# Optimization experiments

Measured on AMD Instinct MI355X. Metric: run time of the kernel, lower is better.

## Reference

```python
import jax, jax.numpy as jnp
import numpy as np

B, SQ, SKV = 4, 2048, 2048
IN_Q, IN_KV = 1024, 1024
H, D = 16, 64            # num_heads, hidden_channels (per-head dim)
OUT = 1024
ROPE_BASE = 4096.0


def _rope(x, base):
    # x: (..., items, D). Interleaved rotate-half RoPE over last dim.
    d = x.shape[-1]
    s = x.shape[-2]
    inv_freq = base ** (-jnp.arange(0, d, 2, dtype=x.dtype) / d)      # (D/2,)
    ang = jnp.arange(s, dtype=x.dtype)[:, None] * inv_freq[None, :]   # (S, D/2)
    cos = jnp.repeat(jnp.cos(ang), 2, axis=-1)                        # (S, D)
    sin = jnp.repeat(jnp.sin(ang), 2, axis=-1)
    xp = x.reshape(x.shape[:-1] + (d // 2, 2))
    x_rot = jnp.stack([-xp[..., 1], xp[..., 0]], axis=-1).reshape(x.shape)
    return x * cos + x_rot * sin


def setup_inputs() -> dict:
    key = jax.random.key(0)
    ks = jax.random.split(key, 8)
    sc = 0.02
    return {
        "q": jax.random.normal(ks[0], (B, SQ, IN_Q), jnp.float32),
        "kv": jax.random.normal(ks[1], (B, SKV, IN_KV), jnp.float32),
        # weights stored (in, out): y = x @ W + b  (equiv. to torch Linear)
        "Wq": jax.random.normal(ks[2], (IN_Q, H * D), jnp.float32) * sc,
        "bq": jnp.zeros((H * D,), jnp.float32),
        "Wkv": jax.random.normal(ks[3], (IN_KV, 2 * D), jnp.float32) * sc,
        "bkv": jnp.zeros((2 * D,), jnp.float32),
        "Wo": jax.random.normal(ks[4], (H * D, OUT), jnp.float32) * sc,
        "bo": jnp.zeros((OUT,), jnp.float32),
    }


def reference(q, kv, Wq, bq, Wkv, bkv, Wo, bo):
    # Q projection -> (B, H, SQ, D)
    qh = (q @ Wq + bq).reshape(B, SQ, H, D).transpose(0, 2, 1, 3)
    # KV projection (multi-query: single shared K/V head) -> (B, SKV, D) each
    kvp = kv @ Wkv + bkv
    k, v = kvp[..., :D], kvp[..., D:]
    # Rotary positional encoding on the item axis
    qh = _rope(qh, ROPE_BASE)
    k = _rope(k, ROPE_BASE)
    # Scaled dot-product attention with broadcast single-head K/V (MQA)
    scale = 1.0 / jnp.sqrt(jnp.asarray(D, qh.dtype))
    scores = jnp.einsum("bhqd,bkd->bhqk", qh, k) * scale   # (B,H,SQ,SKV)
    attn = jax.nn.softmax(scores, axis=-1)
    h = jnp.einsum("bhqk,bkd->bhqd", attn, v)              # (B,H,SQ,D)
    # Merge heads and output projection
    h = h.transpose(0, 2, 1, 3).reshape(B, SQ, H * D)
    return h @ Wo + bo
```

## Files before the change

kernel.cpp:

```cpp
#include <hip/hip_runtime.h>
#include <math.h>

typedef __bf16 bf16;
typedef __bf16 bf16x4 __attribute__((ext_vector_type(4)));
typedef __bf16 bf16x8 __attribute__((ext_vector_type(8)));
typedef float floatx4 __attribute__((ext_vector_type(4)));

#define MFMA16(a, b, c) __builtin_amdgcn_mfma_f32_16x16x32_bf16(a, b, c, 0, 0, 0)

#if __has_builtin(__builtin_amdgcn_exp2f)
#define EXP2F(x) __builtin_amdgcn_exp2f(x)
#else
#define EXP2F(x) exp2f(x)
#endif

constexpr int Bc = 4, SQc = 2048, SKVc = 2048, Hc = 16, Dc = 64;
#define QSCALE 0.18033688011112042f

__device__ __forceinline__ void glds16(const bf16* g, bf16* lds_base, int lane) {
#if __has_builtin(__builtin_amdgcn_global_load_lds)
  __builtin_amdgcn_global_load_lds(
      (const __attribute__((address_space(1))) void*)g,
      (__attribute__((address_space(3))) void*)lds_base, 16, 0, 0);
#else
  *(bf16x8*)(lds_base + 8 * lane) = *(const bf16x8*)g;
#endif
}

__global__ void cvt_bf16(const float* __restrict__ in, bf16* __restrict__ out) {
  const size_t i = ((size_t)blockIdx.x * 256 + threadIdx.x) * 4;
  const float4 v = *(const float4*)&in[i];
  bf16x4 o = {(bf16)v.x, (bf16)v.y, (bf16)v.z, (bf16)v.w};
  *(bf16x4*)&out[i] = o;
}

__global__ void rope_tab_build(float2* __restrict__ tab) {
  const int i = blockIdx.x * 256 + threadIdx.x;
  const int pos = i >> 5, f = i & 31;
  const float ang = (float)pos * exp2f(-0.375f * (float)f);
  float sn, cs;
  sincosf(ang, &sn, &cs);
  tab[i] = make_float2(cs, sn);
}

__global__ void transpose_cvt(const float* __restrict__ in, bf16* __restrict__ out,
                              int K, int N) {
  __shared__ bf16 T[64][72];
  const int tid = threadIdx.x;
  const int n0 = blockIdx.x * 64, k0 = blockIdx.y * 64;
  const int tr = tid >> 4, tc4 = (tid & 15) * 4;
#pragma unroll
  for (int i = 0; i < 4; i++) {
    const int k = tr + 16 * i;
    const float4 v = *(const float4*)&in[(size_t)(k0 + k) * N + n0 + tc4];
    T[tc4 + 0][k] = (bf16)v.x;
    T[tc4 + 1][k] = (bf16)v.y;
    T[tc4 + 2][k] = (bf16)v.z;
    T[tc4 + 3][k] = (bf16)v.w;
  }
  __syncthreads();
  const int nr = tid >> 2, kc = (tid & 3) * 8;
#pragma unroll
  for (int hf = 0; hf < 2; hf++)
    *(bf16x8*)&out[(size_t)(n0 + nr) * K + k0 + kc + 32 * hf] =
        *(const bf16x8*)&T[nr][kc + 32 * hf];
}

__device__ __forceinline__ void gemm_kloop(const bf16* __restrict__ A,
                                           const bf16* __restrict__ BT, int m0,
                                           int n0, int tid, int wave, int lane,
                                           int m, int g, bf16 (*As)[128 * 64],
                                           bf16 (*Bs)[128 * 64],
                                           floatx4 (*acc)[4], int mq, int nq) {
  const int r_ = tid >> 3, p_ = tid & 7;
  const bf16* pA[4];
  const bf16* pB[4];
#pragma unroll
  for (int q = 0; q < 4; q++) {
    const int r = r_ + q * 32;
    const int s = p_ ^ (r & 7);
    pA[q] = &A[(size_t)(m0 + r) * 1024 + 8 * s];
    pB[q] = &BT[(size_t)(n0 + r) * 1024 + 8 * s];
  }

#pragma unroll
  for (int q = 0; q < 4; q++) {
    glds16(pA[q], &As[0][(q * 4 + wave) * 512], lane);
    glds16(pB[q], &Bs[0][(q * 4 + wave) * 512], lane);
  }
  __syncthreads();

  for (int t = 0; t < 16; ++t) {
    const int cur = t & 1;
    if (t < 15) {
      const int k0 = 64 * (t + 1);
#pragma unroll
      for (int q = 0; q < 4; q++) {
        glds16(pA[q] + k0, &As[cur ^ 1][(q * 4 + wave) * 512], lane);
        glds16(pB[q] + k0, &Bs[cur ^ 1][(q * 4 + wave) * 512], lane);
      }
    }
    bf16x8 bb[4][2];
#pragma unroll
    for (int j = 0; j < 4; j++) {
      const int row = nq + 16 * j + m;
#pragma unroll
      for (int kh = 0; kh < 2; kh++)
        bb[j][kh] =
            *(const bf16x8*)&Bs[cur][row * 64 + 8 * ((g + 4 * kh) ^ (row & 7))];
    }
#pragma unroll
    for (int i = 0; i < 4; i++) {
      const int row = mq + 16 * i + m;
      const bf16x8 a0 = *(const bf16x8*)&As[cur][row * 64 + 8 * (g ^ (row & 7))];
      const bf16x8 a1 =
          *(const bf16x8*)&As[cur][row * 64 + 8 * ((g + 4) ^ (row & 7))];
#pragma unroll
      for (int j = 0; j < 4; j++) {
        acc[i][j] = MFMA16(a0, bb[j][0], acc[i][j]);
        acc[i][j] = MFMA16(a1, bb[j][1], acc[i][j]);
      }
    }
    __syncthreads();
  }
}

__global__ __launch_bounds__(256, 2) void gemm_qkv(
    const bf16* __restrict__ qA, const bf16* __restrict__ qBT,
    const float* __restrict__ qb, const bf16* __restrict__ kvA,
    const bf16* __restrict__ kvBT, const float* __restrict__ kvb,
    const float2* __restrict__ tab, bf16* __restrict__ qh,
    bf16* __restrict__ kko, bf16* __restrict__ vto) {
  __shared__ bf16 As[2][128 * 64];
  __shared__ bf16 Bs[2][128 * 64];

  const int tid = threadIdx.x, lane = tid & 63, wave = tid >> 6;
  const int m = lane & 15, g = lane >> 4;
  const int m0 = blockIdx.x * 128;
  const bool isQ = (blockIdx.y < 8);
  const int n0 = isQ ? blockIdx.y * 128 : 0;
  const bf16* A = isQ ? qA : kvA;
  const bf16* BT = isQ ? qBT : kvBT;
  const float* bias = isQ ? qb : kvb;
  const int mq = (wave >> 1) * 64, nq = (wave & 1) * 64;

  floatx4 z = {0.f, 0.f, 0.f, 0.f};
  floatx4 acc[4][4];
#pragma unroll
  for (int i = 0; i < 4; i++)
#pragma unroll
    for (int j = 0; j < 4; j++) acc[i][j] = z;

  gemm_kloop(A, BT, m0, n0, tid, wave, lane, m, g, As, Bs, acc, mq, nq);

  const int rq = 4 * g;
#pragma unroll
  for (int j = 0; j < 4; j++) {
    const int col = n0 + nq + 16 * j + m;
    const float bv = bias[col];
#pragma unroll
    for (int i = 0; i < 4; i++) {
#pragma unroll
      for (int r = 0; r < 4; r++) {
        const int row = m0 + mq + 16 * i + rq + r;
        float v = acc[i][j][r] + bv;
        const float vp = __shfl_xor(v, 1);
        if (isQ) {
          const int d = col & 63, hh = col >> 6;
          const int pos = row & (SQc - 1), b = row >> 11;
          const float2 cssn = tab[pos * 32 + (d >> 1)];
          const float res = (d & 1) ? (v * cssn.x + vp * cssn.y)
                                    : (v * cssn.x - vp * cssn.y);
          qh[(((size_t)(b * Hc + hh) * SQc) + pos) * Dc + d] = (bf16)(res * QSCALE);
        } else {
          const int pos = row & (SKVc - 1), b = row >> 11;
          const size_t fb = (size_t)b * (SKVc * Dc);
          if (col < 64) {
            const int d = col;
            const float2 cssn = tab[pos * 32 + (d >> 1)];
            const float res = (d & 1) ? (v * cssn.x + vp * cssn.y)
                                      : (v * cssn.x - vp * cssn.y);
            const int kc = (pos >> 4) * 2 + (d >> 5);
            const int kl = ((d >> 3) & 3) * 16 + (pos & 15);
            kko[fb + (size_t)kc * 512 + kl * 8 + (d & 7)] = (bf16)res;
          } else {
            const int d = col - 64;
            const int vc = (pos >> 6) * 8 + (d >> 4) * 2 + ((pos >> 5) & 1);
            const int vl = ((pos >> 3) & 3) * 16 + (d & 15);
            vto[fb + (size_t)vc * 512 + vl * 8 + (pos & 7)] = (bf16)v;
          }
        }
      }
    }
  }
}

__global__ __launch_bounds__(256, 2) void gemm_out(
    const bf16* __restrict__ A, const bf16* __restrict__ BT,
    const float* __restrict__ bias, float* __restrict__ out) {
  __shared__ bf16 As[2][128 * 64];
  __shared__ bf16 Bs[2][128 * 64];

  const int tid = threadIdx.x, lane = tid & 63, wave = tid >> 6;
  const int m = lane & 15, g = lane >> 4;
  const int m0 = blockIdx.x * 128, n0 = blockIdx.y * 128;
  const int mq = (wave >> 1) * 64, nq = (wave & 1) * 64;

  floatx4 z = {0.f, 0.f, 0.f, 0.f};
  floatx4 acc[4][4];
#pragma unroll
  for (int i = 0; i < 4; i++)
#pragma unroll
    for (int j = 0; j < 4; j++) acc[i][j] = z;

  gemm_kloop(A, BT, m0, n0, tid, wave, lane, m, g, As, Bs, acc, mq, nq);

  const int rq = 4 * g;
#pragma unroll
  for (int j = 0; j < 4; j++) {
    const int col = n0 + nq + 16 * j + m;
    const float bv = bias[col];
#pragma unroll
    for (int i = 0; i < 4; i++)
#pragma unroll
      for (int r = 0; r < 4; r++) {
        const int row = m0 + mq + 16 * i + rq + r;
        out[(size_t)row * 1024 + col] = acc[i][j][r] + bv;
      }
  }
}

__global__ __launch_bounds__(256, 2) void attn_v5(
    const bf16* __restrict__ qh, const bf16* __restrict__ kk,
    const bf16* __restrict__ vt, bf16* __restrict__ hout) {
  const int bid = blockIdx.x;
  const int qt = bid & 7, h = (bid >> 3) & 15, b = bid >> 7;
  const int tid = threadIdx.x, lane = tid & 63, wave = tid >> 6;
  const int m = lane & 15, g = lane >> 4;

  __shared__ bf16 Pb[4][4][16][68];

  const int q0 = qt * 256 + wave * 64;
  const bf16* qp = qh + (((size_t)(b * Hc + h) * SQc) + q0 + m) * Dc + 8 * g;
  bf16x8 bq[4][2];
#pragma unroll
  for (int s = 0; s < 4; s++) {
    bq[s][0] = *(const bf16x8*)(qp + (size_t)(16 * s) * Dc);
    bq[s][1] = *(const bf16x8*)(qp + (size_t)(16 * s) * Dc + 32);
  }

  const bf16 one = (bf16)1.0f;
  const bf16x8 ones = {one, one, one, one, one, one, one, one};

  floatx4 z = {0.f, 0.f, 0.f, 0.f};
  floatx4 accO[4][4];
  floatx4 lacc[4] = {z, z, z, z};
#pragma unroll
  for (int s = 0; s < 4; s++)
#pragma unroll
    for (int t = 0; t < 4; t++) accO[s][t] = z;

  const bf16* kfb = kk + (size_t)b * (SKVc * Dc) + 8 * lane;
  const bf16* vfb = vt + (size_t)b * (SKVc * Dc) + 8 * lane;

  bf16x8 kf[4][2];
#pragma unroll
  for (int c = 0; c < 4; c++) {
    kf[c][0] = *(const bf16x8*)(kfb + (size_t)(2 * c + 0) * 512);
    kf[c][1] = *(const bf16x8*)(kfb + (size_t)(2 * c + 1) * 512);
  }

  for (int it = 0; it < 32; ++it) {
    bf16x8 vf[4][2];
#pragma unroll
    for (int t = 0; t < 4; t++) {
      vf[t][0] = *(const bf16x8*)(vfb + (size_t)(it * 8 + 2 * t + 0) * 512);
      vf[t][1] = *(const bf16x8*)(vfb + (size_t)(it * 8 + 2 * t + 1) * 512);
    }
    bf16x8 kn[4][2];
    if (it + 1 < 32) {
#pragma unroll
      for (int c = 0; c < 4; c++) {
        kn[c][0] = *(const bf16x8*)(kfb + (size_t)((it + 1) * 8 + 2 * c + 0) * 512);
        kn[c][1] = *(const bf16x8*)(kfb + (size_t)((it + 1) * 8 + 2 * c + 1) * 512);
      }
    }
#pragma unroll
    for (int s = 0; s < 4; s++) {
#pragma unroll
      for (int c = 0; c < 4; c++) {
        floatx4 sv = MFMA16(kf[c][0], bq[s][0], z);
        sv = MFMA16(kf[c][1], bq[s][1], sv);
        bf16x4 pk = {(bf16)EXP2F(sv[0]), (bf16)EXP2F(sv[1]), (bf16)EXP2F(sv[2]),
                     (bf16)EXP2F(sv[3])};
        *(bf16x4*)&Pb[wave][s][m][16 * c + 4 * g] = pk;
      }
    }
#pragma unroll
    for (int s = 0; s < 4; s++) {
      const bf16x8 pa0 = *(const bf16x8*)&Pb[wave][s][m][8 * g];
      const bf16x8 pa1 = *(const bf16x8*)&Pb[wave][s][m][32 + 8 * g];
      lacc[s] = MFMA16(pa0, ones, lacc[s]);
      lacc[s] = MFMA16(pa1, ones, lacc[s]);
#pragma unroll
      for (int t = 0; t < 4; t++) {
        accO[s][t] = MFMA16(pa0, vf[t][0], accO[s][t]);
        accO[s][t] = MFMA16(pa1, vf[t][1], accO[s][t]);
      }
    }
#pragma unroll
    for (int c = 0; c < 4; c++) {
      kf[c][0] = kn[c][0];
      kf[c][1] = kn[c][1];
    }
  }

#pragma unroll
  for (int s = 0; s < 4; s++) {
    floatx4 inv;
#pragma unroll
    for (int r = 0; r < 4; r++) inv[r] = 1.0f / lacc[s][r];
#pragma unroll
    for (int t = 0; t < 4; t++)
#pragma unroll
      for (int r = 0; r < 4; r++) {
        const int qrow = q0 + 16 * s + 4 * g + r;
        hout[((size_t)(b * SQc + qrow)) * (Hc * Dc) + h * Dc + 16 * t + m] =
            (bf16)(accO[s][t][r] * inv[r]);
      }
  }
}

extern "C" void kernel_launch(void* const* d_in, const int* in_sizes, int n_in,
                              void* d_out, int out_size, void* d_ws, size_t ws_size,
                              hipStream_t stream) {
  const float* q = (const float*)d_in[0];
  const float* kv = (const float*)d_in[1];
  const float* Wq = (const float*)d_in[2];
  const float* bq = (const float*)d_in[3];
  const float* Wkv = (const float*)d_in[4];
  const float* bkv = (const float*)d_in[5];
  const float* Wo = (const float*)d_in[6];
  const float* bo = (const float*)d_in[7];

  char* ws = (char*)d_ws;
  bf16* qbf = (bf16*)ws;
  bf16* kvbf = (bf16*)(ws + ((size_t)16 << 20));
  bf16* WqT = (bf16*)(ws + ((size_t)32 << 20));
  bf16* WkvT = (bf16*)(ws + ((size_t)34 << 20));
  float2* rtab = (float2*)(ws + ((size_t)34 << 20) + ((size_t)256 << 10));
  bf16* WoT = (bf16*)(ws + ((size_t)35 << 20));
  bf16* qh = (bf16*)(ws + ((size_t)37 << 20));
  bf16* kk = (bf16*)(ws + ((size_t)53 << 20));
  bf16* vt = (bf16*)(ws + ((size_t)54 << 20));
  bf16* hh = qbf;

  const int M = Bc * SQc;

  rope_tab_build<<<256, 256, 0, stream>>>(rtab);
  cvt_bf16<<<M, 256, 0, stream>>>(q, qbf);
  cvt_bf16<<<M, 256, 0, stream>>>(kv, kvbf);
  transpose_cvt<<<dim3(16, 16), 256, 0, stream>>>(Wq, WqT, 1024, 1024);
  transpose_cvt<<<dim3(2, 16), 256, 0, stream>>>(Wkv, WkvT, 1024, 128);
  transpose_cvt<<<dim3(16, 16), 256, 0, stream>>>(Wo, WoT, 1024, 1024);

  gemm_qkv<<<dim3(64, 9), 256, 0, stream>>>(qbf, WqT, bq, kvbf, WkvT, bkv, rtab,
                                            qh, kk, vt);
  attn_v5<<<Bc * Hc * (SQc / 256), 256, 0, stream>>>(qh, kk, vt, hh);
  gemm_out<<<dim3(64, 8), 256, 0, stream>>>(hh, WoT, bo, (float*)d_out);
}
```

Measured before the change: 289.9 us.

## Stage shared K/V tiles in LDS with async loads across 8 waves

The attention kernel now uses 512 threads (8 waves, 32 query rows each) and loads K (double-buffered) and V tiles cooperatively into shared memory via global_load_lds. Before, each wave read the full K/V tiles straight from global memory into registers. Staging them cuts redundant global/L2 traffic and register pressure, which should allow higher occupancy. The cost is extra block-wide barriers per iteration and less per-wave work to amortize each K fragment.

```diff
diff --git a/kernel.cpp b/kernel.cpp
--- a/kernel.cpp
+++ b/kernel.cpp
@@ -230,7 +230,7 @@
   }
 }
 
-__global__ __launch_bounds__(256, 2) void attn_v5(
+__global__ __launch_bounds__(512, 4) void attn_v5(
     const bf16* __restrict__ qh, const bf16* __restrict__ kk,
     const bf16* __restrict__ vt, bf16* __restrict__ hout) {
   const int bid = blockIdx.x;
@@ -238,13 +238,15 @@
   const int tid = threadIdx.x, lane = tid & 63, wave = tid >> 6;
   const int m = lane & 15, g = lane >> 4;
 
-  __shared__ bf16 Pb[4][4][16][68];
-
-  const int q0 = qt * 256 + wave * 64;
+  __shared__ bf16 Kb[2][4096];
+  __shared__ bf16 Vb[4096];
+  __shared__ bf16 Pb[8][2][16][68];
+
+  const int q0 = qt * 256 + wave * 32;
   const bf16* qp = qh + (((size_t)(b * Hc + h) * SQc) + q0 + m) * Dc + 8 * g;
-  bf16x8 bq[4][2];
-#pragma unroll
-  for (int s = 0; s < 4; s++) {
+  bf16x8 bq[2][2];
+#pragma unroll
+  for (int s = 0; s < 2; s++) {
     bq[s][0] = *(const bf16x8*)(qp + (size_t)(16 * s) * Dc);
     bq[s][1] = *(const bf16x8*)(qp + (size_t)(16 * s) * Dc + 32);
   }
@@ -253,51 +255,55 @@
   const bf16x8 ones = {one, one, one, one, one, one, one, one};
 
   floatx4 z = {0.f, 0.f, 0.f, 0.f};
-  floatx4 accO[4][4];
-  floatx4 lacc[4] = {z, z, z, z};
-#pragma unroll
-  for (int s = 0; s < 4; s++)
+  floatx4 accO[2][4];
+  floatx4 lacc[2] = {z, z};
+#pragma unroll
+  for (int s = 0; s < 2; s++)
 #pragma unroll
     for (int t = 0; t < 4; t++) accO[s][t] = z;
 
-  const bf16* kfb = kk + (size_t)b * (SKVc * Dc) + 8 * lane;
-  const bf16* vfb = vt + (size_t)b * (SKVc * Dc) + 8 * lane;
-
-  bf16x8 kf[4][2];
-#pragma unroll
-  for (int c = 0; c < 4; c++) {
-    kf[c][0] = *(const bf16x8*)(kfb + (size_t)(2 * c + 0) * 512);
-    kf[c][1] = *(const bf16x8*)(kfb + (size_t)(2 * c + 1) * 512);
-  }
+  const size_t fb = (size_t)b * (SKVc * Dc);
+  const bf16* kg = kk + fb + 8 * lane;
+  const bf16* vg = vt + fb + 8 * lane;
+
+  glds16(kg + (size_t)wave * 512, &Kb[0][wave * 512], lane);
+  __syncthreads();
 
   for (int it = 0; it < 32; ++it) {
-    bf16x8 vf[4][2];
-#pragma unroll
-    for (int t = 0; t < 4; t++) {
-      vf[t][0] = *(const bf16x8*)(vfb + (size_t)(it * 8 + 2 * t + 0) * 512);
-      vf[t][1] = *(const bf16x8*)(vfb + (size_t)(it * 8 + 2 * t + 1) * 512);
-    }
-    bf16x8 kn[4][2];
-    if (it + 1 < 32) {
+    const int cur = it & 1;
+    if (it) __syncthreads();
+    glds16(vg + (size_t)(it * 8 + wave) * 512, &Vb[wave * 512], lane);
+    if (it + 1 < 32)
+      glds16(kg + (size_t)((it + 1) * 8 + wave) * 512, &Kb[cur ^ 1][wave * 512],
+             lane);
+
+    bf16x8 kfr[4][2];
+#pragma unroll
+    for (int c = 0; c < 4; c++) {
+      kfr[c][0] = *(const bf16x8*)&Kb[cur][(2 * c + 0) * 512 + 8 * lane];
+      kfr[c][1] = *(const bf16x8*)&Kb[cur][(2 * c + 1) * 512 + 8 * lane];
+    }
+#pragma unroll
+    for (int s = 0; s < 2; s++) {
 #pragma unroll
       for (int c = 0; c < 4; c++) {
-        kn[c][0] = *(const bf16x8*)(kfb + (size_t)((it + 1) * 8 + 2 * c + 0) * 512);
-        kn[c][1] = *(const bf16x8*)(kfb + (size_t)((it + 1) * 8 + 2 * c + 1) * 512);
-      }
-    }
-#pragma unroll
-    for (int s = 0; s < 4; s++) {
-#pragma unroll
-      for (int c = 0; c < 4; c++) {
-        floatx4 sv = MFMA16(kf[c][0], bq[s][0], z);
-        sv = MFMA16(kf[c][1], bq[s][1], sv);
+        floatx4 sv = MFMA16(kfr[c][0], bq[s][0], z);
+        sv = MFMA16(kfr[c][1], bq[s][1], sv);
         bf16x4 pk = {(bf16)EXP2F(sv[0]), (bf16)EXP2F(sv[1]), (bf16)EXP2F(sv[2]),
                      (bf16)EXP2F(sv[3])};
         *(bf16x4*)&Pb[wave][s][m][16 * c + 4 * g] = pk;
       }
     }
-#pragma unroll
-    for (int s = 0; s < 4; s++) {
+    __syncthreads();
+
+    bf16x8 vf[4][2];
+#pragma unroll
+    for (int t = 0; t < 4; t++) {
+      vf[t][0] = *(const bf16x8*)&Vb[(2 * t + 0) * 512 + 8 * lane];
+      vf[t][1] = *(const bf16x8*)&Vb[(2 * t + 1) * 512 + 8 * lane];
+    }
+#pragma unroll
+    for (int s = 0; s < 2; s++) {
       const bf16x8 pa0 = *(const bf16x8*)&Pb[wave][s][m][8 * g];
       const bf16x8 pa1 = *(const bf16x8*)&Pb[wave][s][m][32 + 8 * g];
       lacc[s] = MFMA16(pa0, ones, lacc[s]);
@@ -308,15 +314,10 @@
         accO[s][t] = MFMA16(pa1, vf[t][1], accO[s][t]);
       }
     }
-#pragma unroll
-    for (int c = 0; c < 4; c++) {
-      kf[c][0] = kn[c][0];
-      kf[c][1] = kn[c][1];
-    }
-  }
-
-#pragma unroll
-  for (int s = 0; s < 4; s++) {
+  }
+
+#pragma unroll
+  for (int s = 0; s < 2; s++) {
     floatx4 inv;
 #pragma unroll
     for (int r = 0; r < 4; r++) inv[r] = 1.0f / lacc[s][r];
@@ -366,6 +367,6 @@
 
   gemm_qkv<<<dim3(64, 9), 256, 0, stream>>>(qbf, WqT, bq, kvbf, WkvT, bkv, rtab,
                                             qh, kk, vt);
-  attn_v5<<<Bc * Hc * (SQc / 256), 256, 0, stream>>>(qh, kk, vt, hh);
+  attn_v5<<<Bc * Hc * (SQc / 256), 512, 0, stream>>>(qh, kk, vt, hh);
   gemm_out<<<dim3(64, 8), 256, 0, stream>>>(hh, WoT, bo, (float*)d_out);
 }
```

Result: no change. 284.9 us (-1.7%).
